# Kernel optimization log

Measured on AMD Instinct MI355X. Metric: run time of the kernel, lower is better.

Reference implementation:

```python
import jax, jax.numpy as jnp
import numpy as np

B, T, C = 4, 1024, 1024
H, HKV, D = 16, 4, 64
GATE_CH = 12
ROPE_THETA = 10000.0


def _rms_norm(x):
    # F.rms_norm with default eps = machine epsilon of dtype, no learnable scale
    eps = jnp.finfo(x.dtype).eps
    ms = jnp.mean(jnp.square(x), axis=-1, keepdims=True)
    return x * jax.lax.rsqrt(ms + eps)


def _apply_rotary(x, cos, sin):
    # x: (B, T, h, D); cos/sin: (1, T, 1, D//2). Half-split rotation.
    d = x.shape[-1] // 2
    x1, x2 = x[..., :d], x[..., d:]
    y1 = x1 * cos + x2 * sin
    y2 = -x1 * sin + x2 * cos
    return jnp.concatenate([y1, y2], axis=-1)


def setup_inputs() -> dict:
    key = jax.random.key(0)
    ks = jax.random.split(key, 8)
    x = jax.random.normal(ks[0], (B, T, C), dtype=jnp.float32)
    ve = jax.random.normal(ks[1], (B, T, HKV * D), dtype=jnp.float32)
    # real RoPE tables, shape (1, T, 1, D//2)
    half = D // 2
    inv_freq = 1.0 / (ROPE_THETA ** (np.arange(half, dtype=np.float32) / half))
    freqs = np.arange(T, dtype=np.float32)[:, None] * inv_freq[None, :]
    cos = jnp.asarray(np.cos(freqs), dtype=jnp.float32).reshape(1, T, 1, half)
    sin = jnp.asarray(np.sin(freqs), dtype=jnp.float32).reshape(1, T, 1, half)
    s = 0.02
    Wq = jax.random.normal(ks[2], (H * D, C), dtype=jnp.float32) * s
    Wk = jax.random.normal(ks[3], (HKV * D, C), dtype=jnp.float32) * s
    Wv = jax.random.normal(ks[4], (HKV * D, C), dtype=jnp.float32) * s
    Wo = jax.random.normal(ks[5], (C, C), dtype=jnp.float32) * s
    Wg = jax.random.normal(ks[6], (HKV, GATE_CH), dtype=jnp.float32) * s
    return {"x": x, "ve": ve, "cos": cos, "sin": sin,
            "Wq": Wq, "Wk": Wk, "Wv": Wv, "Wo": Wo, "Wg": Wg,
            "window_size": 256}


def reference(x, ve, cos, sin, Wq, Wk, Wv, Wo, Wg, window_size):
    b, t, c = x.shape
    d = 2 * cos.shape[-1]
    h = Wq.shape[0] // d
    hkv = Wk.shape[0] // d
    rep = h // hkv

    q = (x @ Wq.T).reshape(b, t, h, d)
    k = (x @ Wk.T).reshape(b, t, hkv, d)
    v = (x @ Wv.T).reshape(b, t, hkv, d)

    # value-embedding sigmoid gate (3 * sigmoid of first 12 channels of x)
    gate = 3.0 * jax.nn.sigmoid(x[..., : Wg.shape[1]] @ Wg.T)  # (b, t, hkv)
    v = v + gate[..., None] * ve.reshape(b, t, hkv, d)

    q = _apply_rotary(q, cos, sin)
    k = _apply_rotary(k, cos, sin)
    q = _rms_norm(q) * 1.2
    k = _rms_norm(k) * 1.2

    # GQA attention with sliding-window causal mask (left=window_size, right=0)
    qg = q.reshape(b, t, hkv, rep, d)
    scale = 1.0 / jnp.sqrt(jnp.asarray(d, dtype=q.dtype))
    scores = jnp.einsum('bqgrd,bkgd->bgrqk', qg, k) * scale
    i = jnp.arange(t)[:, None]
    j = jnp.arange(t)[None, :]
    mask = (j <= i) & ((i - j) <= window_size)  # (t, t)
    scores = jnp.where(mask[None, None, None], scores, -jnp.inf)
    probs = jax.nn.softmax(scores, axis=-1)
    y = jnp.einsum('bgrqk,bkgd->bqgrd', probs, v).reshape(b, t, h * d)
    return y @ Wo.T
```

## Files before the change

kernel.cpp:

```cpp
#include <hip/hip_runtime.h>

typedef __bf16 v8bf __attribute__((ext_vector_type(8)));
typedef float v4f __attribute__((ext_vector_type(4)));
typedef unsigned int v4u __attribute__((ext_vector_type(4)));
typedef unsigned int v2u __attribute__((ext_vector_type(2)));
typedef unsigned short u16;

#define DEVI static __device__ __forceinline__

DEVI float bf2f(u16 u) {
    union { float f; unsigned int i; } c; c.i = ((unsigned int)u) << 16; return c.f;
}
DEVI u16 f2bf(float f) {
    union { __bf16 b; u16 u; } c; c.b = (__bf16)f;
    return c.u;
}

union Frag { v4u u; v8bf v; u16 h[8]; };

#define GLD16(gptr, lptr) __builtin_amdgcn_global_load_lds( \
    (const __attribute__((address_space(1))) void*)(gptr),  \
    (__attribute__((address_space(3))) void*)(lptr), 16, 0, 0)

#define BAR_VM8()  asm volatile("s_waitcnt vmcnt(8)\ns_barrier" ::: "memory")
#define BAR_VM6()  asm volatile("s_waitcnt vmcnt(6)\ns_barrier" ::: "memory")
#define BAR_VM0()  asm volatile("s_waitcnt vmcnt(0)\ns_barrier" ::: "memory")
#define BAR_LGKM() asm volatile("s_waitcnt lgkmcnt(0)\ns_barrier" ::: "memory")

__global__ __launch_bounds__(256) void convert6(
    const float* __restrict__ x, const float* __restrict__ wq,
    const float* __restrict__ wk, const float* __restrict__ wv,
    const float* __restrict__ wo, const float* __restrict__ Wg,
    u16* __restrict__ xb, u16* __restrict__ wb, u16* __restrict__ wob,
    float* __restrict__ gates)
{
    if (blockIdx.y == 5) {
        const int stride = gridDim.x * 256;
        for (int i = blockIdx.x * 256 + threadIdx.x; i < 4096 * 4; i += stride) {
            const int token = i >> 2, g = i & 3;
            float dot = 0.f;
#pragma unroll
            for (int c = 0; c < 12; c++)
                dot += x[token * 1024 + c] * Wg[g * 12 + c];
            gates[i] = 3.f / (1.f + __expf(-dot));
        }
        return;
    }
    const float* src; u16* dst; int n;
    switch (blockIdx.y) {
        case 0: src = x;  dst = xb;               n = 4096 * 1024; break;
        case 1: src = wq; dst = wb;               n = 1024 * 1024; break;
        case 2: src = wk; dst = wb + 1024 * 1024; n = 256 * 1024;  break;
        case 3: src = wv; dst = wb + 1280 * 1024; n = 256 * 1024;  break;
        default: src = wo; dst = wob;             n = 1024 * 1024; break;
    }
    const int stride = gridDim.x * 256 * 4;
    for (int i = (blockIdx.x * 256 + threadIdx.x) * 4; i < n; i += stride) {
        const float4 f = *(const float4*)(src + i);
        v2u p;
        p[0] = (unsigned int)f2bf(f.x) | ((unsigned int)f2bf(f.y) << 16);
        p[1] = (unsigned int)f2bf(f.z) | ((unsigned int)f2bf(f.w) << 16);
        *(v2u*)(dst + i) = p;
    }
}

__global__ __launch_bounds__(256) void gemm_qkv(
    const u16* __restrict__ A, const u16* __restrict__ B,
    const float* __restrict__ cs, const float* __restrict__ sn,
    const float* __restrict__ gates, const float* __restrict__ ve,
    u16* __restrict__ qn, u16* __restrict__ kn, u16* __restrict__ vt)
{
    __shared__ __align__(16) u16 As[2][128 * 64];
    __shared__ __align__(16) u16 Bs[2][128 * 64];
    const int tid  = threadIdx.x;
    const int lane = tid & 63, l15 = lane & 15, quad = (lane >> 4) & 3;
    const int w    = tid >> 6;
    const int wr   = (w >> 1) * 64, wc = (w & 1) * 64;
    const int m0   = blockIdx.x * 128, n0 = blockIdx.y * 128;

    const int r0 = tid >> 3;
    const int c0 = (tid & 7) * 8;
    const u16* ag = A + m0 * 1024 + r0 * 1024 + c0;
    const u16* bg = B + n0 * 1024 + r0 * 1024 + c0;
    const int lo = r0 * 64 + c0;

    v4f acc[4][4];
    const v4f vzero = {0.f, 0.f, 0.f, 0.f};
#pragma unroll
    for (int i = 0; i < 4; i++)
#pragma unroll
        for (int j = 0; j < 4; j++) acc[i][j] = vzero;

#define QKV_STAGE(k0, buf) {                                        \
        const u16* a_ = ag + (k0);  const u16* b_ = bg + (k0);      \
        u16* al_ = &As[buf][lo];    u16* bl_ = &Bs[buf][lo];        \
        GLD16(a_,             al_);                                 \
        GLD16(a_ + 32 * 1024, al_ + 32 * 64);                       \
        GLD16(a_ + 64 * 1024, al_ + 64 * 64);                       \
        GLD16(a_ + 96 * 1024, al_ + 96 * 64);                       \
        GLD16(b_,             bl_);                                 \
        GLD16(b_ + 32 * 1024, bl_ + 32 * 64);                       \
        GLD16(b_ + 64 * 1024, bl_ + 64 * 64);                       \
        GLD16(b_ + 96 * 1024, bl_ + 96 * 64);                       \
    }

    QKV_STAGE(0, 0);
    for (int t = 0; t < 16; ++t) {
        if (t < 15) {
            QKV_STAGE((t + 1) * 64, (t + 1) & 1);
            BAR_VM8();
        } else {
            BAR_VM0();
        }
        const u16* Asb = As[t & 1];
        const u16* Bsb = Bs[t & 1];
#pragma unroll
        for (int ks = 0; ks < 2; ks++) {
            v8bf af[4], bv[4];
#pragma unroll
            for (int mi = 0; mi < 4; mi++)
                af[mi] = *(const v8bf*)&Asb[(wr + mi * 16 + l15) * 64 + ks * 32 + quad * 8];
#pragma unroll
            for (int ni = 0; ni < 4; ni++)
                bv[ni] = *(const v8bf*)&Bsb[(wc + ni * 16 + l15) * 64 + ks * 32 + quad * 8];
#pragma unroll
            for (int ni = 0; ni < 4; ni++)
#pragma unroll
                for (int mi = 0; mi < 4; mi++)
                    acc[mi][ni] = __builtin_amdgcn_mfma_f32_16x16x32_bf16(af[mi], bv[ni], acc[mi][ni], 0, 0, 0);
        }
        BAR_LGKM();
    }
#undef QKV_STAGE

    const int hcol = n0 + wc;
    if (hcol < 1280) {
        const bool isQ = (hcol < 1024);
        u16* dst = isQ ? (qn + (hcol >> 6) * 64) : (kn + ((hcol - 1024) >> 6) * 64);
        const int dstride = isQ ? 1024 : 256;
#pragma unroll
        for (int mi = 0; mi < 4; mi++) {
#pragma unroll
            for (int r = 0; r < 4; r++) {
                const int row = m0 + wr + mi * 16 + quad * 4 + r;
                const int pos = row & 1023;
                const float c0_ = cs[pos * 32 + l15],      s0_ = sn[pos * 32 + l15];
                const float c1_ = cs[pos * 32 + 16 + l15], s1_ = sn[pos * 32 + 16 + l15];
                const float y0 = acc[mi][0][r] * c0_ + acc[mi][2][r] * s0_;
                const float y2 = acc[mi][2][r] * c0_ - acc[mi][0][r] * s0_;
                const float y1 = acc[mi][1][r] * c1_ + acc[mi][3][r] * s1_;
                const float y3 = acc[mi][3][r] * c1_ - acc[mi][1][r] * s1_;
                float ss = y0 * y0 + y1 * y1 + y2 * y2 + y3 * y3;
#pragma unroll
                for (int off = 8; off >= 1; off >>= 1)
                    ss += __shfl_xor(ss, off, 64);
                const float inv = rsqrtf(ss * (1.0f / 64.0f) + 1.1920929e-7f) * 1.2f;
                u16* d = dst + row * dstride;
                d[l15]      = f2bf(y0 * inv);
                d[16 + l15] = f2bf(y1 * inv);
                d[32 + l15] = f2bf(y2 * inv);
                d[48 + l15] = f2bf(y3 * inv);
            }
        }
    } else {
        const int g = (hcol - 1280) >> 6;
#pragma unroll
        for (int mi = 0; mi < 4; mi++) {
            const int row0 = m0 + wr + mi * 16 + quad * 4;
            const int b_ = row0 >> 10, t_ = row0 & 1023;
            float gate[4];
#pragma unroll
            for (int r = 0; r < 4; r++) gate[r] = gates[(row0 + r) * 4 + g];
#pragma unroll
            for (int ni = 0; ni < 4; ni++) {
                const int d = ni * 16 + l15;
                union { u16 h[4]; v2u u; } pk;
#pragma unroll
                for (int r = 0; r < 4; r++)
                    pk.h[r] = f2bf(acc[mi][ni][r] + gate[r] * ve[(row0 + r) * 256 + g * 64 + d]);
                *(v2u*)&vt[((b_ * 4 + g) * 64 + d) * 1024 + t_] = pk.u;
            }
        }
    }
}

__global__ __launch_bounds__(256) void gemm_out(
    const u16* __restrict__ A, const u16* __restrict__ B,
    float* __restrict__ C, int N)
{
    __shared__ __align__(16) u16 As[2][64 * 64];
    __shared__ __align__(16) u16 Bs[2][128 * 64];
    const int tid  = threadIdx.x;
    const int lane = tid & 63, l15 = lane & 15, quad = (lane >> 4) & 3;
    const int w    = tid >> 6;
    const int wr   = (w >> 1) * 32, wc = (w & 1) * 64;
    const int m0   = blockIdx.x * 64, n0 = blockIdx.y * 128;

    const int r0 = tid >> 3;
    const int c0 = (tid & 7) * 8;
    const u16* ag = A + m0 * 1024 + r0 * 1024 + c0;
    const u16* bg = B + n0 * 1024 + r0 * 1024 + c0;
    const int lo = r0 * 64 + c0;

    v4f acc[2][4];
    const v4f vzero = {0.f, 0.f, 0.f, 0.f};
#pragma unroll
    for (int i = 0; i < 2; i++)
#pragma unroll
        for (int j = 0; j < 4; j++) acc[i][j] = vzero;

#define OUT_STAGE(k0, buf) {                                        \
        const u16* a_ = ag + (k0);  const u16* b_ = bg + (k0);      \
        u16* al_ = &As[buf][lo];    u16* bl_ = &Bs[buf][lo];        \
        GLD16(a_,             al_);                                 \
        GLD16(a_ + 32 * 1024, al_ + 32 * 64);                       \
        GLD16(b_,             bl_);                                 \
        GLD16(b_ + 32 * 1024, bl_ + 32 * 64);                       \
        GLD16(b_ + 64 * 1024, bl_ + 64 * 64);                       \
        GLD16(b_ + 96 * 1024, bl_ + 96 * 64);                       \
    }

    OUT_STAGE(0, 0);
    for (int t = 0; t < 16; ++t) {
        if (t < 15) {
            OUT_STAGE((t + 1) * 64, (t + 1) & 1);
            BAR_VM6();
        } else {
            BAR_VM0();
        }
        const u16* Asb = As[t & 1];
        const u16* Bsb = Bs[t & 1];
#pragma unroll
        for (int ks = 0; ks < 2; ks++) {
            v8bf af[2];
#pragma unroll
            for (int mi = 0; mi < 2; mi++)
                af[mi] = *(const v8bf*)&Asb[(wr + mi * 16 + l15) * 64 + ks * 32 + quad * 8];
#pragma unroll
            for (int ni = 0; ni < 4; ni++) {
                v8bf bv = *(const v8bf*)&Bsb[(wc + ni * 16 + l15) * 64 + ks * 32 + quad * 8];
#pragma unroll
                for (int mi = 0; mi < 2; mi++)
                    acc[mi][ni] = __builtin_amdgcn_mfma_f32_16x16x32_bf16(af[mi], bv, acc[mi][ni], 0, 0, 0);
            }
        }
        BAR_LGKM();
    }
#undef OUT_STAGE

#pragma unroll
    for (int mi = 0; mi < 2; mi++) {
        const int row = m0 + wr + mi * 16 + quad * 4;
#pragma unroll
        for (int ni = 0; ni < 4; ni++) {
            const int col = n0 + wc + ni * 16 + l15;
#pragma unroll
            for (int r = 0; r < 4; r++)
                C[(row + r) * N + col] = acc[mi][ni][r];
        }
    }
}

__global__ __launch_bounds__(256) void attn(
    const u16* __restrict__ qn, const u16* __restrict__ kn,
    const u16* __restrict__ vt, u16* __restrict__ yo)
{
    __shared__ __align__(16) u16 Ks[64 * 72];
    __shared__ __align__(16) u16 VTs[64 * 72];
    __shared__ __align__(16) u16 Ps[4][16 * 72];
    const int tid  = threadIdx.x;
    const int w    = tid >> 6, lane = tid & 63, l15 = lane & 15, quad = (lane >> 4) & 3;
    const int qb   = blockIdx.x, h = blockIdx.y, b = blockIdx.z;
    const int g    = h >> 2;
    const int qbase = qb * 64;
    const int qabs0 = qbase + w * 16;
    const int tok0  = b * 1024 + qabs0;
    u16* pw = Ps[w];

    v8bf qf[2];
#pragma unroll
    for (int ks = 0; ks < 2; ks++) {
        Frag f;
        f.u = *(const v4u*)&qn[(tok0 + l15) * 1024 + h * 64 + ks * 32 + quad * 8];
#pragma unroll
        for (int j = 0; j < 8; j++) f.h[j] = f2bf(0.18033688f * bf2f(f.h[j]));
        qf[ks] = f.v;
    }

    v4f o[4];
    float li[4];
    const v4f vzero = {0.f, 0.f, 0.f, 0.f};
#pragma unroll
    for (int nd = 0; nd < 4; nd++) o[nd] = vzero;
#pragma unroll
    for (int r = 0; r < 4; r++) li[r] = 0.f;

    const int row = tid >> 2, ch = (tid & 3) * 16;
    const int kstart = (qbase >= 256) ? qbase - 256 : 0;
    const int kend   = qbase;

    v4u ka, kb, va, vb;
#define LOADKV(kb_)  {                                                        \
        const int goff_ = (b * 1024 + (kb_) + row) * 256 + g * 64 + ch;       \
        ka = *(const v4u*)&kn[goff_];                                         \
        kb = *(const v4u*)&kn[goff_ + 8];                                     \
        const u16* vs_ = vt + ((b * 4 + g) * 64 + row) * 1024 + (kb_) + ch;   \
        va = *(const v4u*)vs_;                                                \
        vb = *(const v4u*)(vs_ + 8);                                          \
    }

    LOADKV(kstart);
    for (int kbase = kstart; kbase <= kend; kbase += 64) {
        *(v4u*)&Ks[row * 72 + ch]      = ka;
        *(v4u*)&Ks[row * 72 + ch + 8]  = kb;
        *(v4u*)&VTs[row * 72 + ch]     = va;
        *(v4u*)&VTs[row * 72 + ch + 8] = vb;
        if (kbase + 64 <= kend) LOADKV(kbase + 64);
        BAR_LGKM();

        bool skip2[4], full2[4];
#pragma unroll
        for (int ni = 0; ni < 4; ni++) {
            const int left = kbase + ni * 16;
            skip2[ni] = (left > qabs0 + 15) || (qabs0 - (left + 15) > 256);
            full2[ni] = ((left + 15) <= qabs0) && ((qabs0 + 15 - left) <= 256);
        }

#pragma unroll
        for (int ni = 0; ni < 4; ni++) {
            if (skip2[ni]) {
#pragma unroll
                for (int r = 0; r < 4; r++)
                    pw[(quad * 4 + r) * 72 + ni * 16 + l15] = 0;
                continue;
            }
            v8bf kf0 = *(const v8bf*)&Ks[(ni * 16 + l15) * 72 + quad * 8];
            v8bf kf1 = *(const v8bf*)&Ks[(ni * 16 + l15) * 72 + 32 + quad * 8];
            v4f a = vzero;
            a = __builtin_amdgcn_mfma_f32_16x16x32_bf16(qf[0], kf0, a, 0, 0, 0);
            a = __builtin_amdgcn_mfma_f32_16x16x32_bf16(qf[1], kf1, a, 0, 0, 0);
            if (!full2[ni]) {
                const int kj = kbase + ni * 16 + l15;
#pragma unroll
                for (int r = 0; r < 4; r++) {
                    const int qi = qabs0 + quad * 4 + r;
                    if (!((kj <= qi) && (qi - kj <= 256))) a[r] = -1e30f;
                }
            }
#pragma unroll
            for (int r = 0; r < 4; r++) {
                const float p = exp2f(a[r] - 17.312340f);
                li[r] += p;
                pw[(quad * 4 + r) * 72 + ni * 16 + l15] = f2bf(p);
            }
        }

#pragma unroll
        for (int ks = 0; ks < 2; ks++) {
            if (skip2[2 * ks] && skip2[2 * ks + 1]) continue;
            v8bf af = *(const v8bf*)&pw[l15 * 72 + ks * 32 + quad * 8];
#pragma unroll
            for (int nd = 0; nd < 4; nd++) {
                v8bf bv = *(const v8bf*)&VTs[(nd * 16 + l15) * 72 + ks * 32 + quad * 8];
                o[nd] = __builtin_amdgcn_mfma_f32_16x16x32_bf16(af, bv, o[nd], 0, 0, 0);
            }
        }
        BAR_LGKM();
    }
#undef LOADKV

#pragma unroll
    for (int off = 8; off >= 1; off >>= 1)
#pragma unroll
        for (int r = 0; r < 4; r++)
            li[r] += __shfl_xor(li[r], off, 64);
    float inv[4];
#pragma unroll
    for (int r = 0; r < 4; r++) inv[r] = 1.f / li[r];
#pragma unroll
    for (int nd = 0; nd < 4; nd++) {
        const int col = h * 64 + nd * 16 + l15;
#pragma unroll
        for (int r = 0; r < 4; r++) {
            const int row2 = tok0 + quad * 4 + r;
            yo[row2 * 1024 + col] = f2bf(o[nd][r] * inv[r]);
        }
    }
}

extern "C" void kernel_launch(void* const* d_in, const int* in_sizes, int n_in,
                              void* d_out, int out_size, void* d_ws, size_t ws_size,
                              hipStream_t stream)
{
    const float* x  = (const float*)d_in[0];
    const float* ve = (const float*)d_in[1];
    const float* cs = (const float*)d_in[2];
    const float* sn = (const float*)d_in[3];
    const float* Wq = (const float*)d_in[4];
    const float* Wk = (const float*)d_in[5];
    const float* Wv = (const float*)d_in[6];
    const float* Wo = (const float*)d_in[7];
    const float* Wg = (const float*)d_in[8];

    u16*   xb    = (u16*)d_ws;
    u16*   wb    = xb  + 4096 * 1024;
    u16*   wob   = wb  + 1536 * 1024;
    u16*   qn    = wob + 1024 * 1024;
    u16*   kn    = qn  + 4096 * 1024;
    u16*   vt    = kn  + 4096 * 256;
    u16*   ay    = vt  + 4096 * 256;
    float* gates = (float*)(ay + 4096 * 1024);

    convert6<<<dim3(512, 6), 256, 0, stream>>>(x, Wq, Wk, Wv, Wo, Wg, xb, wb, wob, gates);
    gemm_qkv<<<dim3(32, 12), 256, 0, stream>>>(xb, wb, cs, sn, gates, ve, qn, kn, vt);
    attn<<<dim3(16, 16, 4), 256, 0, stream>>>(qn, kn, vt, ay);
    gemm_out<<<dim3(64, 8), 256, 0, stream>>>(ay, wob, (float*)d_out, 1024);
}
```

Baseline: 156.8 us.

## Double-buffer K tiles in LDS and read V fragments directly from global

The attention kernel keeps two K tile buffers in shared memory and writes the next tile after computing on the current one. This removes the trailing barrier from each key-block iteration. V is no longer staged in shared memory: each lane loads its PV-MFMA operand straight from the transposed V in global memory, with rows 1024 elements apart. This cuts LDS traffic and a sync, but each wave now issues its own strided global V loads, and all four waves redundantly read the same V data, relying on caches.

```diff
diff --git a/kernel.cpp b/kernel.cpp
--- a/kernel.cpp
+++ b/kernel.cpp
@@ -265,8 +265,7 @@
     const u16* __restrict__ qn, const u16* __restrict__ kn,
     const u16* __restrict__ vt, u16* __restrict__ yo)
 {
-    __shared__ __align__(16) u16 Ks[64 * 72];
-    __shared__ __align__(16) u16 VTs[64 * 72];
+    __shared__ __align__(16) u16 Ks[2][64 * 72];
     __shared__ __align__(16) u16 Ps[4][16 * 72];
     const int tid  = threadIdx.x;
     const int w    = tid >> 6, lane = tid & 63, l15 = lane & 15, quad = (lane >> 4) & 3;
@@ -298,24 +297,24 @@
     const int row = tid >> 2, ch = (tid & 3) * 16;
     const int kstart = (qbase >= 256) ? qbase - 256 : 0;
     const int kend   = qbase;
-
-    v4u ka, kb, va, vb;
-#define LOADKV(kb_)  {                                                        \
+    const u16* vrow0 = vt + ((b * 4 + g) * 64) * 1024;
+
+    v4u ka, kb;
+#define LOADK(kb_)  {                                                         \
         const int goff_ = (b * 1024 + (kb_) + row) * 256 + g * 64 + ch;       \
         ka = *(const v4u*)&kn[goff_];                                         \
         kb = *(const v4u*)&kn[goff_ + 8];                                     \
-        const u16* vs_ = vt + ((b * 4 + g) * 64 + row) * 1024 + (kb_) + ch;   \
-        va = *(const v4u*)vs_;                                                \
-        vb = *(const v4u*)(vs_ + 8);                                          \
-    }
-
-    LOADKV(kstart);
-    for (int kbase = kstart; kbase <= kend; kbase += 64) {
-        *(v4u*)&Ks[row * 72 + ch]      = ka;
-        *(v4u*)&Ks[row * 72 + ch + 8]  = kb;
-        *(v4u*)&VTs[row * 72 + ch]     = va;
-        *(v4u*)&VTs[row * 72 + ch + 8] = vb;
-        if (kbase + 64 <= kend) LOADKV(kbase + 64);
+    }
+
+    LOADK(kstart);
+    *(v4u*)&Ks[0][row * 72 + ch]     = ka;
+    *(v4u*)&Ks[0][row * 72 + ch + 8] = kb;
+
+    int t = 0;
+    for (int kbase = kstart; kbase <= kend; kbase += 64, ++t) {
+        const int cur = t & 1;
+        const bool more = (kbase + 64 <= kend);
+        if (more) LOADK(kbase + 64);
         BAR_LGKM();
 
         bool skip2[4], full2[4];
@@ -326,6 +325,7 @@
             full2[ni] = ((left + 15) <= qabs0) && ((qabs0 + 15 - left) <= 256);
         }
 
+        const u16* Kc = Ks[cur];
 #pragma unroll
         for (int ni = 0; ni < 4; ni++) {
             if (skip2[ni]) {
@@ -334,8 +334,8 @@
                     pw[(quad * 4 + r) * 72 + ni * 16 + l15] = 0;
                 continue;
             }
-            v8bf kf0 = *(const v8bf*)&Ks[(ni * 16 + l15) * 72 + quad * 8];
-            v8bf kf1 = *(const v8bf*)&Ks[(ni * 16 + l15) * 72 + 32 + quad * 8];
+            v8bf kf0 = *(const v8bf*)&Kc[(ni * 16 + l15) * 72 + quad * 8];
+            v8bf kf1 = *(const v8bf*)&Kc[(ni * 16 + l15) * 72 + 32 + quad * 8];
             v4f a = vzero;
             a = __builtin_amdgcn_mfma_f32_16x16x32_bf16(qf[0], kf0, a, 0, 0, 0);
             a = __builtin_amdgcn_mfma_f32_16x16x32_bf16(qf[1], kf1, a, 0, 0, 0);
@@ -359,15 +359,21 @@
         for (int ks = 0; ks < 2; ks++) {
             if (skip2[2 * ks] && skip2[2 * ks + 1]) continue;
             v8bf af = *(const v8bf*)&pw[l15 * 72 + ks * 32 + quad * 8];
+            const u16* vb_ = vrow0 + kbase + ks * 32 + quad * 8;
 #pragma unroll
             for (int nd = 0; nd < 4; nd++) {
-                v8bf bv = *(const v8bf*)&VTs[(nd * 16 + l15) * 72 + ks * 32 + quad * 8];
+                v8bf bv = *(const v8bf*)&vb_[(nd * 16 + l15) * 1024];
                 o[nd] = __builtin_amdgcn_mfma_f32_16x16x32_bf16(af, bv, o[nd], 0, 0, 0);
             }
         }
-        BAR_LGKM();
-    }
-#undef LOADKV
+
+        if (more) {
+            u16* kd = &Ks[cur ^ 1][row * 72 + ch];
+            *(v4u*)kd       = ka;
+            *(v4u*)(kd + 8) = kb;
+        }
+    }
+#undef LOADK
 
 #pragma unroll
     for (int off = 8; off >= 1; off >>= 1)
```

Measured after the change: 163.9 us. 4.5% more time.
